# Kernel tuning notes

Hardware: AMD Instinct MI355X
Metric: run time of the kernel (lower is better)

Reference implementation:

```python
import jax, jax.numpy as jnp
import numpy as np
import math

IN_CH, KEY_SIZE, VALUE_SIZE = 512, 64, 64
N, T = 4, 4096

def setup_inputs() -> dict:
    key = jax.random.key(0)
    ks = jax.random.split(key, 7)
    s_in = 1.0 / math.sqrt(IN_CH)
    return {
        "x": jax.random.normal(ks[0], (N, T, IN_CH), dtype=jnp.float32),
        "Wq": jax.random.uniform(ks[1], (IN_CH, KEY_SIZE), jnp.float32, -s_in, s_in),
        "bq": jax.random.uniform(ks[2], (KEY_SIZE,), jnp.float32, -s_in, s_in),
        "Wk": jax.random.uniform(ks[3], (IN_CH, KEY_SIZE), jnp.float32, -s_in, s_in),
        "bk": jax.random.uniform(ks[4], (KEY_SIZE,), jnp.float32, -s_in, s_in),
        "Wv": jax.random.uniform(ks[5], (IN_CH, VALUE_SIZE), jnp.float32, -s_in, s_in),
        "bv": jax.random.uniform(ks[6], (VALUE_SIZE,), jnp.float32, -s_in, s_in),
    }

def reference(x, Wq, bq, Wk, bk, Wv, bv):
    # x: [N, T, C]
    Tlen = x.shape[1]
    q = x @ Wq + bq              # [N, T, K]
    k = x @ Wk + bk              # [N, T, K]
    v = x @ Wv + bv              # [N, T, V]
    logits = jnp.einsum('ntk,nsk->nts', q, k)  # [N, T, T]
    # causal mask: strict upper triangle -> -inf (applied BEFORE scaling, as in the original)
    causal = jnp.tril(jnp.ones((Tlen, Tlen), dtype=bool))
    logits = jnp.where(causal, logits, -jnp.inf)
    scale = 1.0 / math.sqrt(Wq.shape[1])
    attn = jax.nn.softmax(logits * scale, axis=-1)
    read = jnp.einsum('nts,nsv->ntv', attn, v)  # [N, T, V]
    return jnp.concatenate((x, read), axis=2)   # [N, T, C+V]
```

## Files before the change

kernel.cpp:

```cpp
#include <hip/hip_runtime.h>
#include <stdint.h>

typedef __attribute__((ext_vector_type(8))) short bf16x8;
typedef __attribute__((ext_vector_type(4))) float f32x4;
typedef __attribute__((ext_vector_type(4))) unsigned short u16x4;
typedef unsigned short u16;

#define NBATCH 4
#define SEQ    4096
#define CIN    512
#define HD     64
#define OC     576
#define NROW   (NBATCH * SEQ)

__device__ __forceinline__ float b2f(u16 u) {
    union { uint32_t i; float f; } w; w.i = ((uint32_t)u) << 16; return w.f;
}
__device__ __forceinline__ u16 f2b(float f) {
    union { float f; uint32_t i; } w; w.f = f;
    uint32_t r = w.i + 0x7fffu + ((w.i >> 16) & 1u);
    return (u16)(r >> 16);
}
__device__ __forceinline__ uint32_t cvtpk_bf16(float a, float b) {
    uint32_t r;
    asm("v_cvt_pk_bf16_f32 %0, %1, %2" : "=v"(r) : "v"(a), "v"(b));
    return r;
}

__global__ void prep_wt(const float* __restrict__ Wq, const float* __restrict__ Wk,
                        const float* __restrict__ Wv, u16* __restrict__ wt) {
    int row = blockIdx.x;
    int g = row >> 6, j = row & 63;
    const float* W = (g == 0) ? Wq : (g == 1) ? Wk : Wv;
    for (int k = threadIdx.x; k < CIN; k += blockDim.x)
        wt[row * CIN + k] = f2b(W[k * HD + j]);
}

__global__ __launch_bounds__(256) void proj(
    const float* __restrict__ x, const u16* __restrict__ wt,
    const float* __restrict__ bq, const float* __restrict__ bk, const float* __restrict__ bv,
    u16* __restrict__ qb, u16* __restrict__ kbuf, u16* __restrict__ vtb,
    float* __restrict__ out)
{
    __shared__ __align__(16) float xs[32 * 512];

    int tid = threadIdx.x;
    int lane = tid & 63, w = tid >> 6;
    int m = lane & 15, quad = lane >> 4;
    int r0b = blockIdx.x * 32;

    {
        int rw = w >> 1;
        int pp = (w & 1) * 64 + lane;
#pragma unroll
        for (int k = 0; k < 16; k++) {
            int r = k * 2 + rw;
            int g = pp ^ (r & 15);
            const float* src = x + (size_t)(r0b + r) * CIN + g * 4;
            float* dst = xs + (size_t)(k * 256 + w * 64 + lane) * 4;
            __builtin_amdgcn_global_load_lds(
                (const __attribute__((address_space(1))) void*)src,
                (__attribute__((address_space(3))) void*)dst, 16, 0, 0);
        }
    }
    __syncthreads();

    int tile = blockIdx.x * 2 + (w >> 1);
    int half = w & 1;
    int r0 = tile * 16;
    int ntb = half * 6;

    f32x4 acc[6];
#pragma unroll
    for (int i = 0; i < 6; i++) acc[i] = (f32x4){0.f, 0.f, 0.f, 0.f};

    const float* xrow = xs + (size_t)((w >> 1) * 16 + m) * 512;

#pragma unroll
    for (int c = 0; c < 16; c++) {
        int L0 = c * 8 + quad * 2;
        f32x4 va = *(const f32x4*)(xrow + (size_t)((L0 ^ m) * 4));
        f32x4 vb = *(const f32x4*)(xrow + (size_t)(((L0 + 1) ^ m) * 4));
        bf16x8 a;
#pragma unroll
        for (int j = 0; j < 4; j++) { a[j] = (short)f2b(va[j]); a[4 + j] = (short)f2b(vb[j]); }
#pragma unroll
        for (int t = 0; t < 6; t++) {
            int nt = ntb + t;
            bf16x8 b = *(const bf16x8*)(wt + (size_t)(nt * 16 + m) * CIN + c * 32 + quad * 8);
            acc[t] = __builtin_amdgcn_mfma_f32_16x16x32_bf16(a, b, acc[t], 0, 0, 0);
        }
    }

#pragma unroll
    for (int k = 0; k < 16; k++) {
        int G = k * 256 + tid;
        int r = G >> 7, p = G & 127;
        f32x4 v = *(const f32x4*)(xs + (size_t)G * 4);
        int col = (p ^ (r & 15)) * 4;
        *(f32x4*)(out + (size_t)(r0b + r) * OC + col) = v;
    }

    int n  = r0 >> 12;
    int tl = r0 & (SEQ - 1);

    const float SCQ = 0.125f * 1.44269504088896f;

    if (half == 0) {
#pragma unroll
        for (int t = 0; t < 4; t++) {
            int bi = t * 16 + m;
            float biasq = bq[bi];
#pragma unroll
            for (int reg = 0; reg < 4; reg++) {
                size_t r = (size_t)(r0 + quad * 4 + reg);
                qb[r * HD + bi] = f2b((acc[t][reg] + biasq) * SCQ);
            }
        }
#pragma unroll
        for (int t = 4; t < 6; t++) {
            int bi = (t - 4) * 16 + m;
            float biask = bk[bi];
#pragma unroll
            for (int reg = 0; reg < 4; reg++) {
                size_t r = (size_t)(r0 + quad * 4 + reg);
                kbuf[r * HD + bi] = f2b(acc[t][reg] + biask);
            }
        }
    } else {
#pragma unroll
        for (int t = 0; t < 2; t++) {
            int bi = (t + 2) * 16 + m;
            float biask = bk[bi];
#pragma unroll
            for (int reg = 0; reg < 4; reg++) {
                size_t r = (size_t)(r0 + quad * 4 + reg);
                kbuf[r * HD + bi] = f2b(acc[t][reg] + biask);
            }
        }
#pragma unroll
        for (int t = 2; t < 6; t++) {
            int bi = (t - 2) * 16 + m;
            float biasv = bv[bi];
            u16x4 pk;
#pragma unroll
            for (int reg = 0; reg < 4; reg++) pk[reg] = f2b(acc[t][reg] + biasv);
            u16* vp = vtb + (size_t)(n * HD + bi) * SEQ + tl + quad * 4;
            *(u16x4*)vp = pk;
        }
    }
}

__global__ __launch_bounds__(512, 2) void attn(
    const u16* __restrict__ qb, const u16* __restrict__ kbuf,
    const u16* __restrict__ vtb, float* __restrict__ out)
{
    __shared__ __align__(16) union {
        short p[8][16 * 72];
        float o[8][16][68];
    } lu;
    __shared__ float ldsm[8][16];
    __shared__ float ldsl[8][16];

    int tid = threadIdx.x;
    int lane = tid & 63, w = tid >> 6;
    int m = lane & 15, quad = lane >> 4;

    int idx = blockIdx.x;
    int xcd = idx & 7;
    int batch = xcd >> 1;
    int sub = (idx >> 3) * 2 + (xcd & 1);
    int jj = 127 - sub;
    int t0 = jj * 32;
    int nkb = (jj >> 1) + 1;
    int lastkb = nkb - 1;

    const u16* kp = kbuf + (size_t)(batch * SEQ + m) * HD + quad * 8;
    const u16* vp = vtb + (size_t)(batch * HD + m) * SEQ + quad * 8;

    bf16x8 ones;
#pragma unroll
    for (int i = 0; i < 8; i++) ones[i] = (short)0x3F80;

    const u16* qpb = qb + (size_t)(batch * SEQ + t0 + m) * HD + quad * 8;
    bf16x8 q0[2], q1[2];
#pragma unroll
    for (int q = 0; q < 2; q++) {
        q0[q] = *(const bf16x8*)(qpb + (size_t)(q * 16) * HD);
        q1[q] = *(const bf16x8*)(qpb + (size_t)(q * 16) * HD + 32);
    }

    float mst[2];
    f32x4 o[2][4], ol[2];
#pragma unroll
    for (int q = 0; q < 2; q++) {
        mst[q] = -1e30f;
        ol[q] = (f32x4){0.f, 0.f, 0.f, 0.f};
#pragma unroll
        for (int nt = 0; nt < 4; nt++) o[q][nt] = (f32x4){0.f, 0.f, 0.f, 0.f};
    }

    int cnt = (nkb > w) ? ((nkb - w + 7) >> 3) : 0;
    int kb = w;
    short* pw = &lu.p[w][0];

    bf16x8 k0[4], k1[4];
#pragma unroll
    for (int st = 0; st < 4; st++) {
        k0[st] = *(const bf16x8*)(kp + (size_t)(kb * 64 + st * 16) * HD);
        k1[st] = *(const bf16x8*)(kp + (size_t)(kb * 64 + st * 16) * HD + 32);
    }

    for (int it = 0; it < cnt; it++, kb += 8) {
        int s0 = kb * 64;
        bool diag = (kb == lastkb);

        bf16x8 vf0[4], vf1[4];
#pragma unroll
        for (int nt = 0; nt < 4; nt++) {
            vf0[nt] = *(const bf16x8*)(vp + (size_t)(nt * 16) * SEQ + s0);
            vf1[nt] = *(const bf16x8*)(vp + (size_t)(nt * 16) * SEQ + s0 + 32);
        }

        f32x4 s[2][4];
#pragma unroll
        for (int q = 0; q < 2; q++)
#pragma unroll
            for (int st = 0; st < 4; st++) {
                f32x4 a = (f32x4){0.f, 0.f, 0.f, 0.f};
                a = __builtin_amdgcn_mfma_f32_16x16x32_bf16(k0[st], q0[q], a, 0, 0, 0);
                a = __builtin_amdgcn_mfma_f32_16x16x32_bf16(k1[st], q1[q], a, 0, 0, 0);
                s[q][st] = a;
            }

        if (it + 1 < cnt) {
            int sn = s0 + 512;
#pragma unroll
            for (int st = 0; st < 4; st++) {
                k0[st] = *(const bf16x8*)(kp + (size_t)(sn + st * 16) * HD);
                k1[st] = *(const bf16x8*)(kp + (size_t)(sn + st * 16) * HD + 32);
            }
        }

        if (diag) {
#pragma unroll
            for (int q = 0; q < 2; q++)
#pragma unroll
                for (int st = 0; st < 4; st++)
#pragma unroll
                    for (int r = 0; r < 4; r++) {
                        int key = s0 + st * 16 + quad * 4 + r;
                        if (key > t0 + q * 16 + m) s[q][st][r] = -1e30f;
                    }
        }

        bf16x8 pf0[2], pf1[2];
#pragma unroll
        for (int q = 0; q < 2; q++) {
            float mx = -1e30f;
#pragma unroll
            for (int st = 0; st < 4; st++) {
                float a01 = fmaxf(s[q][st][0], s[q][st][1]);
                float a23 = fmaxf(s[q][st][2], s[q][st][3]);
                mx = fmaxf(mx, fmaxf(a01, a23));
            }
            mx = fmaxf(mx, __shfl_xor(mx, 16, 64));
            mx = fmaxf(mx, __shfl_xor(mx, 32, 64));

            if (__any(mx > mst[q] + 8.0f)) {
                float mn = fmaxf(mst[q], mx);
                float al = exp2f(mst[q] - mn);
#pragma unroll
                for (int nt = 0; nt < 4; nt++)
#pragma unroll
                    for (int r = 0; r < 4; r++) o[q][nt][r] *= al;
                ol[q][0] *= al;
                mst[q] = mn;
            }

#pragma unroll
            for (int st = 0; st < 4; st++) {
                float e0 = exp2f(s[q][st][0] - mst[q]);
                float e1 = exp2f(s[q][st][1] - mst[q]);
                float e2 = exp2f(s[q][st][2] - mst[q]);
                float e3 = exp2f(s[q][st][3] - mst[q]);
                uint2 pk2;
                pk2.x = cvtpk_bf16(e0, e1);
                pk2.y = cvtpk_bf16(e2, e3);
                *(uint2*)(pw + m * 72 + st * 16 + quad * 4) = pk2;
            }
            __asm__ volatile("" ::: "memory");
            pf0[q] = *(const bf16x8*)(pw + m * 72 + quad * 8);
            pf1[q] = *(const bf16x8*)(pw + m * 72 + 32 + quad * 8);
            __asm__ volatile("" ::: "memory");
        }

#pragma unroll
        for (int q = 0; q < 2; q++) {
#pragma unroll
            for (int nt = 0; nt < 4; nt++) {
                o[q][nt] = __builtin_amdgcn_mfma_f32_16x16x32_bf16(vf0[nt], pf0[q], o[q][nt], 0, 0, 0);
                o[q][nt] = __builtin_amdgcn_mfma_f32_16x16x32_bf16(vf1[nt], pf1[q], o[q][nt], 0, 0, 0);
            }
            ol[q] = __builtin_amdgcn_mfma_f32_16x16x32_bf16(ones, pf0[q], ol[q], 0, 0, 0);
            ol[q] = __builtin_amdgcn_mfma_f32_16x16x32_bf16(ones, pf1[q], ol[q], 0, 0, 0);
        }
    }

    __syncthreads();

#pragma unroll
    for (int q = 0; q < 2; q++) {
        if (quad == 0) { ldsm[w][m] = mst[q]; ldsl[w][m] = ol[q][0]; }
#pragma unroll
        for (int nt = 0; nt < 4; nt++)
            *(f32x4*)&lu.o[w][m][nt * 16 + quad * 4] = o[q][nt];
        __syncthreads();

        if (tid < 256) {
            int t = tid >> 4, vg = tid & 15;
            float mmax = -1e30f;
#pragma unroll
            for (int u = 0; u < 8; u++) mmax = fmaxf(mmax, ldsm[u][t]);
            float L = 0.f;
            f32x4 acc = (f32x4){0.f, 0.f, 0.f, 0.f};
#pragma unroll
            for (int u = 0; u < 8; u++) {
                float c = exp2f(ldsm[u][t] - mmax);
                L += ldsl[u][t] * c;
                f32x4 ov = *(const f32x4*)&lu.o[u][t][vg * 4];
#pragma unroll
                for (int i2 = 0; i2 < 4; i2++) acc[i2] += ov[i2] * c;
            }
            float inv = 1.0f / L;
            f32x4 res;
#pragma unroll
            for (int i2 = 0; i2 < 4; i2++) res[i2] = acc[i2] * inv;
            *(f32x4*)(out + (size_t)(batch * SEQ + t0 + q * 16 + t) * OC + CIN + vg * 4) = res;
        }
        __syncthreads();
    }
}

extern "C" void kernel_launch(void* const* d_in, const int* in_sizes, int n_in,
                              void* d_out, int out_size, void* d_ws, size_t ws_size,
                              hipStream_t stream) {
    const float* x  = (const float*)d_in[0];
    const float* Wq = (const float*)d_in[1];
    const float* bq = (const float*)d_in[2];
    const float* Wk = (const float*)d_in[3];
    const float* bk = (const float*)d_in[4];
    const float* Wv = (const float*)d_in[5];
    const float* bv = (const float*)d_in[6];
    float* out = (float*)d_out;

    u16* ws  = (u16*)d_ws;
    u16* wt  = ws;
    u16* qb  = ws + 131072;
    u16* kb  = qb + 16384 * 64;
    u16* vtb = kb + 16384 * 64;

    prep_wt<<<dim3(192), dim3(256), 0, stream>>>(Wq, Wk, Wv, wt);
    proj<<<dim3(512), dim3(256), 0, stream>>>(x, wt, bq, bk, bv, qb, kb, vtb, out);
    attn<<<dim3(512), dim3(512), 0, stream>>>(qb, kb, vtb, out);
}
```

Baseline: 155.9 us.

## Store K and V in MFMA-fragment-tiled layout and halve projection tile rows

```diff
diff --git a/kernel.cpp b/kernel.cpp
--- a/kernel.cpp
+++ b/kernel.cpp
@@ -12,6 +12,7 @@
 #define HD     64
 #define OC     576
 #define NROW   (NBATCH * SEQ)
+#define KVB    262144
 
 __device__ __forceinline__ float b2f(u16 u) {
     union { uint32_t i; float f; } w; w.i = ((uint32_t)u) << 16; return w.f;
@@ -42,21 +43,21 @@
     u16* __restrict__ qb, u16* __restrict__ kbuf, u16* __restrict__ vtb,
     float* __restrict__ out)
 {
-    __shared__ __align__(16) float xs[32 * 512];
+    __shared__ __align__(16) float xs[16 * 512];
 
     int tid = threadIdx.x;
     int lane = tid & 63, w = tid >> 6;
     int m = lane & 15, quad = lane >> 4;
-    int r0b = blockIdx.x * 32;
+    int r0 = blockIdx.x * 16;
 
     {
         int rw = w >> 1;
         int pp = (w & 1) * 64 + lane;
 #pragma unroll
-        for (int k = 0; k < 16; k++) {
+        for (int k = 0; k < 8; k++) {
             int r = k * 2 + rw;
             int g = pp ^ (r & 15);
-            const float* src = x + (size_t)(r0b + r) * CIN + g * 4;
+            const float* src = x + (size_t)(r0 + r) * CIN + g * 4;
             float* dst = xs + (size_t)(k * 256 + w * 64 + lane) * 4;
             __builtin_amdgcn_global_load_lds(
                 (const __attribute__((address_space(1))) void*)src,
@@ -65,16 +66,13 @@
     }
     __syncthreads();
 
-    int tile = blockIdx.x * 2 + (w >> 1);
-    int half = w & 1;
-    int r0 = tile * 16;
-    int ntb = half * 6;
-
-    f32x4 acc[6];
-#pragma unroll
-    for (int i = 0; i < 6; i++) acc[i] = (f32x4){0.f, 0.f, 0.f, 0.f};
-
-    const float* xrow = xs + (size_t)((w >> 1) * 16 + m) * 512;
+    int ntb = w * 3;
+
+    f32x4 acc[3];
+#pragma unroll
+    for (int i = 0; i < 3; i++) acc[i] = (f32x4){0.f, 0.f, 0.f, 0.f};
+
+    const float* xrow = xs + (size_t)m * 512;
 
 #pragma unroll
     for (int c = 0; c < 16; c++) {
@@ -85,7 +83,7 @@
 #pragma unroll
         for (int j = 0; j < 4; j++) { a[j] = (short)f2b(va[j]); a[4 + j] = (short)f2b(vb[j]); }
 #pragma unroll
-        for (int t = 0; t < 6; t++) {
+        for (int t = 0; t < 3; t++) {
             int nt = ntb + t;
             bf16x8 b = *(const bf16x8*)(wt + (size_t)(nt * 16 + m) * CIN + c * 32 + quad * 8);
             acc[t] = __builtin_amdgcn_mfma_f32_16x16x32_bf16(a, b, acc[t], 0, 0, 0);
@@ -93,12 +91,12 @@
     }
 
 #pragma unroll
-    for (int k = 0; k < 16; k++) {
+    for (int k = 0; k < 8; k++) {
         int G = k * 256 + tid;
         int r = G >> 7, p = G & 127;
         f32x4 v = *(const f32x4*)(xs + (size_t)G * 4);
         int col = (p ^ (r & 15)) * 4;
-        *(f32x4*)(out + (size_t)(r0b + r) * OC + col) = v;
+        *(f32x4*)(out + (size_t)(r0 + r) * OC + col) = v;
     }
 
     int n  = r0 >> 12;
@@ -106,47 +104,35 @@
 
     const float SCQ = 0.125f * 1.44269504088896f;
 
-    if (half == 0) {
-#pragma unroll
-        for (int t = 0; t < 4; t++) {
-            int bi = t * 16 + m;
+#pragma unroll
+    for (int t = 0; t < 3; t++) {
+        int nt = ntb + t;
+        int bi = (nt & 3) * 16 + m;
+        if (nt < 4) {
             float biasq = bq[bi];
 #pragma unroll
             for (int reg = 0; reg < 4; reg++) {
                 size_t r = (size_t)(r0 + quad * 4 + reg);
                 qb[r * HD + bi] = f2b((acc[t][reg] + biasq) * SCQ);
             }
-        }
-#pragma unroll
-        for (int t = 4; t < 6; t++) {
-            int bi = (t - 4) * 16 + m;
+        } else if (nt < 8) {
             float biask = bk[bi];
+            u16* kbase = kbuf + (size_t)n * KVB
+                       + (((size_t)(tl >> 4) * 8 + (bi >> 3)) * 16) * 8 + (bi & 7);
 #pragma unroll
             for (int reg = 0; reg < 4; reg++) {
-                size_t r = (size_t)(r0 + quad * 4 + reg);
-                kbuf[r * HD + bi] = f2b(acc[t][reg] + biask);
-            }
-        }
-    } else {
-#pragma unroll
-        for (int t = 0; t < 2; t++) {
-            int bi = (t + 2) * 16 + m;
-            float biask = bk[bi];
-#pragma unroll
-            for (int reg = 0; reg < 4; reg++) {
-                size_t r = (size_t)(r0 + quad * 4 + reg);
-                kbuf[r * HD + bi] = f2b(acc[t][reg] + biask);
-            }
-        }
-#pragma unroll
-        for (int t = 2; t < 6; t++) {
-            int bi = (t - 2) * 16 + m;
+                int mkey = quad * 4 + reg;
+                kbase[(size_t)mkey * 8] = f2b(acc[t][reg] + biask);
+            }
+        } else {
             float biasv = bv[bi];
             u16x4 pk;
 #pragma unroll
             for (int reg = 0; reg < 4; reg++) pk[reg] = f2b(acc[t][reg] + biasv);
-            u16* vp = vtb + (size_t)(n * HD + bi) * SEQ + tl + quad * 4;
-            *(u16x4*)vp = pk;
+            int key0 = tl + quad * 4;
+            size_t off = ((((size_t)(bi >> 4) * 128 + (key0 >> 5)) * 4
+                           + ((key0 >> 3) & 3)) * 16 + (bi & 15)) * 8 + (key0 & 7);
+            *(u16x4*)(vtb + (size_t)n * KVB + off) = pk;
         }
     }
 }
@@ -175,8 +161,8 @@
     int nkb = (jj >> 1) + 1;
     int lastkb = nkb - 1;
 
-    const u16* kp = kbuf + (size_t)(batch * SEQ + m) * HD + quad * 8;
-    const u16* vp = vtb + (size_t)(batch * HD + m) * SEQ + quad * 8;
+    const u16* kpb = kbuf + (size_t)batch * KVB;
+    const u16* vpb = vtb + (size_t)batch * KVB;
 
     bf16x8 ones;
 #pragma unroll
@@ -207,8 +193,8 @@
     bf16x8 k0[4], k1[4];
 #pragma unroll
     for (int st = 0; st < 4; st++) {
-        k0[st] = *(const bf16x8*)(kp + (size_t)(kb * 64 + st * 16) * HD);
-        k1[st] = *(const bf16x8*)(kp + (size_t)(kb * 64 + st * 16) * HD + 32);
+        k0[st] = *(const bf16x8*)(kpb + (size_t)((kb * 4 + st) * 8 + quad) * 128 + m * 8);
+        k1[st] = *(const bf16x8*)(kpb + (size_t)((kb * 4 + st) * 8 + quad + 4) * 128 + m * 8);
     }
 
     for (int it = 0; it < cnt; it++, kb += 8) {
@@ -218,8 +204,8 @@
         bf16x8 vf0[4], vf1[4];
 #pragma unroll
         for (int nt = 0; nt < 4; nt++) {
-            vf0[nt] = *(const bf16x8*)(vp + (size_t)(nt * 16) * SEQ + s0);
-            vf1[nt] = *(const bf16x8*)(vp + (size_t)(nt * 16) * SEQ + s0 + 32);
+            vf0[nt] = *(const bf16x8*)(vpb + (size_t)((nt * 128 + (s0 >> 5)) * 4 + quad) * 128 + m * 8);
+            vf1[nt] = *(const bf16x8*)(vpb + (size_t)((nt * 128 + (s0 >> 5) + 1) * 4 + quad) * 128 + m * 8);
         }
 
         f32x4 s[2][4];
@@ -234,11 +220,11 @@
             }
 
         if (it + 1 < cnt) {
-            int sn = s0 + 512;
+            int kn = kb + 8;
 #pragma unroll
             for (int st = 0; st < 4; st++) {
-                k0[st] = *(const bf16x8*)(kp + (size_t)(sn + st * 16) * HD);
-                k1[st] = *(const bf16x8*)(kp + (size_t)(sn + st * 16) * HD + 32);
+                k0[st] = *(const bf16x8*)(kpb + (size_t)((kn * 4 + st) * 8 + quad) * 128 + m * 8);
+                k1[st] = *(const bf16x8*)(kpb + (size_t)((kn * 4 + st) * 8 + quad + 4) * 128 + m * 8);
             }
         }
 
@@ -361,6 +347,6 @@
     u16* vtb = kb + 16384 * 64;
 
     prep_wt<<<dim3(192), dim3(256), 0, stream>>>(Wq, Wk, Wv, wt);
-    proj<<<dim3(512), dim3(256), 0, stream>>>(x, wt, bq, bk, bv, qb, kb, vtb, out);
+    proj<<<dim3(1024), dim3(256), 0, stream>>>(x, wt, bq, bk, bv, qb, kb, vtb, out);
     attn<<<dim3(512), dim3(512), 0, stream>>>(qb, kb, vtb, out);
 }
```

Measured after the change: 140.6 us. 1.11x faster.
